# Performance work log

Hardware: AMD Instinct MI355X
Metric: run time of the kernel (lower is better)

## Reference

```python
import jax, jax.numpy as jnp
import numpy as np

N = 20000      # nodes
E = 320000     # edges (before self loops)
HID = 128      # args.hidden
HEADS = 8
C1 = HID // 2  # 64, gat1 out per head -> 512 concat
C2 = HID // 4  # 32, gat2 out per head -> 256 concat
D1 = HEADS * C1  # 512
D2 = HEADS * C2  # 256
JKD = HID + D1 + D2  # 896


def _glorot(key, shape):
    fan_in, fan_out = shape[0], shape[-1]
    s = jnp.sqrt(6.0 / (fan_in + fan_out))
    return jax.random.uniform(key, shape, jnp.float32, -s, s)


def setup_inputs() -> dict:
    key = jax.random.key(0)
    ks = jax.random.split(key, 18)
    x = jax.random.normal(ks[0], (N, HID), jnp.float32)
    edge_index = jax.random.randint(ks[1], (2, E), 0, N, dtype=jnp.int32)
    return {
        "x": x,
        "edge_index": edge_index,
        # GATv2 layer 1
        "Wl1": _glorot(ks[2], (HID, D1)), "bl1": jnp.zeros((D1,), jnp.float32),
        "Wr1": _glorot(ks[3], (HID, D1)), "br1": jnp.zeros((D1,), jnp.float32),
        "att1": _glorot(ks[4], (HEADS, C1)),
        "bias1": jnp.zeros((D1,), jnp.float32),
        # GATv2 layer 2
        "Wl2": _glorot(ks[5], (D1, D2)), "bl2": jnp.zeros((D2,), jnp.float32),
        "Wr2": _glorot(ks[6], (D1, D2)), "br2": jnp.zeros((D2,), jnp.float32),
        "att2": _glorot(ks[7], (HEADS, C2)),
        "bias2": jnp.zeros((D2,), jnp.float32),
        # JK linear
        "Wjk": _glorot(ks[8], (JKD, HID)), "bjk": jnp.zeros((HID,), jnp.float32),
    }


def gatv2_layer(x, src, dst, Wl, bl, Wr, br, att, bias, n):
    """PyG GATv2Conv (concat=True, eval mode: no dropout), neg_slope=0.2."""
    H, C = att.shape
    xl = (x @ Wl + bl).reshape(n, H, C)  # source transform (messages)
    xr = (x @ Wr + br).reshape(n, H, C)  # target transform
    e = jax.nn.leaky_relu(xl[src] + xr[dst], 0.2)        # [E,H,C]
    logits = jnp.einsum('ehc,hc->eh', e, att)            # [E,H]
    # numerically stable segment softmax over incoming edges per dst node
    m = jax.ops.segment_max(logits, dst, num_segments=n) # [N,H]
    a = jnp.exp(logits - m[dst])
    denom = jax.ops.segment_sum(a, dst, num_segments=n)
    alpha = a / denom[dst]                               # [E,H]
    out = jax.ops.segment_sum(alpha[:, :, None] * xl[src], dst, num_segments=n)
    return out.reshape(n, H * C) + bias


def reference(x, edge_index, Wl1, bl1, Wr1, br1, att1, bias1,
              Wl2, bl2, Wr2, br2, att2, bias2, Wjk, bjk):
    n = x.shape[0]
    loop = jnp.arange(n, dtype=edge_index.dtype)
    src = jnp.concatenate([edge_index[0], loop])  # add self loops (PyG default)
    dst = jnp.concatenate([edge_index[1], loop])

    jk0 = x
    h1 = jax.nn.elu(gatv2_layer(x, src, dst, Wl1, bl1, Wr1, br1, att1, bias1, n))
    h2 = jax.nn.elu(gatv2_layer(h1, src, dst, Wl2, bl2, Wr2, br2, att2, bias2, n))
    jk = jnp.concatenate([jk0, h1, h2], axis=-1)  # JumpingKnowledge('cat')
    return jk @ Wjk + bjk
```

## Files before the change

### kernel.cpp

```cpp
#include <hip/hip_runtime.h>

typedef unsigned short u16;
typedef __attribute__((ext_vector_type(8))) short bf16x8;
typedef __attribute__((ext_vector_type(4))) float f32x4;

__device__ __forceinline__ float bf2f(u16 u) { return __uint_as_float(((unsigned)u) << 16); }
__device__ __forceinline__ u16 f2bf(float f) {
  unsigned u = __float_as_uint(f);
  u += 0x7fffu + ((u >> 16) & 1u);
  return (u16)(u >> 16);
}
__device__ __forceinline__ void bf2x2(unsigned w, float& lo, float& hi) {
  lo = __uint_as_float(w << 16);
  hi = __uint_as_float(w & 0xffff0000u);
}

__global__ __launch_bounds__(256) void prep_kernel(
    const float* __restrict__ x,
    const float* __restrict__ bl1, const float* __restrict__ br1,
    const float* __restrict__ bl2, const float* __restrict__ br2,
    u16* __restrict__ XH, float* __restrict__ BC1, float* __restrict__ BC2,
    int nx, int total)
{
  int i = blockIdx.x * 256 + threadIdx.x;
  if (i >= total) return;
  if (i < nx) { XH[i] = f2bf(x[i]); return; }
  int j = i - nx;
  if (j < 1024) { BC1[j] = (j < 512) ? bl1[j] : br1[j - 512]; return; }
  int t = j - 1024;
  BC2[t] = (t < 256) ? bl2[t] : br2[t - 256];
}

__global__ __launch_bounds__(256) void wtrans_kernel(
    const float* __restrict__ Wl1, const float* __restrict__ Wr1,
    const float* __restrict__ Wl2, const float* __restrict__ Wr2,
    const float* __restrict__ Wjk,
    u16* __restrict__ Wp)
{
  __shared__ float T[64][65];
  int t = blockIdx.x;
  const float *Wa, *Wb; int Nhalf, lds, k0, n0, KsT, SUBS; size_t obase; bool split;
  if (t < 32) {
    int kt = t & 1, nt = t >> 1;
    k0 = kt * 64; n0 = nt * 64; obase = 0; KsT = 4; SUBS = 8; split = true;
    Wa = Wl1; Wb = Wr1; Nhalf = 512; lds = 512;
  } else if (t < 96) {
    int tt = t - 32; int kt = tt & 7, nt = tt >> 3;
    k0 = kt * 64; n0 = nt * 64; obase = 262144; KsT = 16; SUBS = 8; split = true;
    Wa = Wl2; Wb = Wr2; Nhalf = 256; lds = 256;
  } else {
    int tt = t - 96; int kt = tt % 14, nt = tt / 14;
    k0 = kt * 64; n0 = nt * 64; obase = 786432; KsT = 28; SUBS = 4; split = false;
    Wa = Wjk; Wb = nullptr; Nhalf = 128; lds = 128;
  }
  const int tid = threadIdx.x;
  const int lane = tid & 63, unit = tid >> 6;
  {
    int n = n0 + lane;
    const float* S = (n < Nhalf) ? Wa : Wb;
    int nn = (n < Nhalf) ? n : n - Nhalf;
#pragma unroll
    for (int r = 0; r < 16; ++r) {
      int kl = unit + 4 * r;
      T[kl][lane] = S[(size_t)(k0 + kl) * lds + nn];
    }
  }
  __syncthreads();
  const int tn = n0 >> 6;
#pragma unroll
  for (int u = 0; u < 2; ++u) {
    int c = unit * 2 + u;
    int ks_l = c >> 2, nc = c & 3;
    int ksg = (k0 >> 5) + ks_l;
    size_t ob = obase + ((size_t)(tn * KsT + ksg) * SUBS + nc) * 512 + lane * 8;
#pragma unroll
    for (int j = 0; j < 8; ++j) {
      float v = T[ks_l * 32 + (lane >> 4) * 8 + j][nc * 16 + (lane & 15)];
      u16 h = f2bf(v);
      Wp[ob + j] = h;
      if (split) Wp[ob + 2048 + j] = f2bf(v - bf2f(h));
    }
  }
}

__global__ __launch_bounds__(256) void hist_kernel(
    const int* __restrict__ ei, int E, int ET, int* __restrict__ cnt)
{
  int e = blockIdx.x * 256 + threadIdx.x;
  if (e >= ET) return;
  int d = (e < E) ? ei[E + e] : (e - E);
  atomicAdd(&cnt[d], 1);
}

__global__ __launch_bounds__(1024) void scan_kernel(
    const int* __restrict__ cnt, int* __restrict__ rowptr, int n)
{
  __shared__ int wsum[16];
  __shared__ int carry;
  const int tid = threadIdx.x, lane = tid & 63, wv = tid >> 6;
  if (tid == 0) carry = 0;
  __syncthreads();
  for (int base = 0; base < n; base += 1024) {
    int i = base + tid;
    int v = (i < n) ? cnt[i] : 0;
    int s = v;
#pragma unroll
    for (int ofs = 1; ofs < 64; ofs <<= 1) {
      int t = __shfl_up(s, ofs);
      if (lane >= ofs) s += t;
    }
    if (lane == 63) wsum[wv] = s;
    __syncthreads();
    if (wv == 0 && lane < 16) {
      int t = wsum[lane];
#pragma unroll
      for (int ofs = 1; ofs < 16; ofs <<= 1) {
        int u = __shfl_up(t, ofs);
        if (lane >= ofs) t += u;
      }
      wsum[lane] = t;
    }
    __syncthreads();
    int waveoff = (wv == 0) ? 0 : wsum[wv - 1];
    if (i < n) rowptr[i] = carry + waveoff + s - v;
    int tot = wsum[15];
    __syncthreads();
    if (tid == 0) carry += tot;
    __syncthreads();
  }
  if (threadIdx.x == 0) rowptr[n] = carry;
}

__global__ __launch_bounds__(256) void scatter_kernel(
    const int* __restrict__ ei, int E, int ET,
    const int* __restrict__ rowptr, int* __restrict__ cur, int* __restrict__ srcs)
{
  int e = blockIdx.x * 256 + threadIdx.x;
  if (e >= ET) return;
  int s, d;
  if (e < E) { s = ei[e]; d = ei[E + e]; } else { s = e - E; d = s; }
  int pos = rowptr[d] + atomicAdd(&cur[d], 1);
  srcs[pos] = s;
}

template<int MROWS, int NW, int WPE, bool SPLIT, bool BF16OUT, int LDSU16>
__global__ __launch_bounds__(NW * 64, WPE) void gemmct_kernel(
    const u16* __restrict__ A0, int lda0, int K0,
    const u16* __restrict__ A1, int lda1, int K1,
    const u16* __restrict__ A2, int lda2, int K2,
    const u16* __restrict__ Wp, int KsT,
    int kof0, int kof1, int kof2,
    const float* __restrict__ bias,
    void* __restrict__ Cv, int ldc, int M, int N)
{
  constexpr int SUBS = SPLIT ? 8 : 4;
  __shared__ u16 ldsA[LDSU16];
  const int tid  = threadIdx.x;
  const int lane = tid & 63;
  const int wv   = tid >> 6;
  const int quad = lane >> 4;
  const int r16  = lane & 15;
  const int m0   = blockIdx.x * MROWS;

  const u16* As[3]   = {A0, A1, A2};
  const int  Ks[3]   = {K0, K1, K2};
  const int  ldas[3] = {lda0, lda1, lda2};
  const int  kofs[3] = {kof0, kof1, kof2};

  int soff[3];
  int so = 0;
#pragma unroll
  for (int s = 0; s < 3; ++s) {
    const int K = Ks[s];
    soff[s] = so;
    if (K == 0) continue;
    const int stride = K + 8;
    const int cpr = K >> 3;
    const int sh  = 32 - __clz(cpr - 1);
    const int tot = MROWS << sh;
    for (int c = tid; c < tot; c += NW * 64) {
      int row = c >> sh, kc = c & ((1 << sh) - 1);
      if (kc < cpr) {
        int sr = m0 + row; if (sr >= M) sr = M - 1;
        uint4 v = *reinterpret_cast<const uint4*>(As[s] + (size_t)sr * ldas[s] + kc * 8);
        *reinterpret_cast<uint4*>(&ldsA[so + row * stride + kc * 8]) = v;
      }
    }
    so += MROWS * stride;
  }
  __syncthreads();

  constexpr int MM = MROWS / 16;
  for (int n0w = wv * 64; n0w < N; n0w += NW * 64) {
    const int t = n0w >> 6;
    f32x4 acc[MM][4];
#pragma unroll
    for (int mm = 0; mm < MM; ++mm)
#pragma unroll
      for (int nc = 0; nc < 4; ++nc) acc[mm][nc] = (f32x4){0.f, 0.f, 0.f, 0.f};

#pragma unroll
    for (int s = 0; s < 3; ++s) {
      const int K = Ks[s];
      if (K == 0) continue;
      const int stride = K + 8;
      const int ksb = kofs[s] >> 5;
      const u16* lbase = &ldsA[soff[s] + r16 * stride + quad * 8];

#pragma unroll 2
      for (int k0 = 0; k0 < K; k0 += 32) {
        const int ks = ksb + (k0 >> 5);
        const u16* ch = Wp + (((size_t)(t * KsT + ks) * SUBS) << 9) + lane * 8;
        bf16x8 af[MM];
#pragma unroll
        for (int mm = 0; mm < MM; ++mm)
          af[mm] = *reinterpret_cast<const bf16x8*>(lbase + mm * 16 * stride + k0);
        bf16x8 whf[4], wlf[4];
#pragma unroll
        for (int nc = 0; nc < 4; ++nc) {
          whf[nc] = *reinterpret_cast<const bf16x8*>(ch + (nc << 9));
          if (SPLIT) wlf[nc] = *reinterpret_cast<const bf16x8*>(ch + ((4 + nc) << 9));
        }
#pragma unroll
        for (int mm = 0; mm < MM; ++mm)
#pragma unroll
          for (int nc = 0; nc < 4; ++nc) {
            acc[mm][nc] = __builtin_amdgcn_mfma_f32_16x16x32_bf16(whf[nc], af[mm], acc[mm][nc], 0, 0, 0);
            if (SPLIT)
              acc[mm][nc] = __builtin_amdgcn_mfma_f32_16x16x32_bf16(wlf[nc], af[mm], acc[mm][nc], 0, 0, 0);
          }
      }
    }

#pragma unroll
    for (int mm = 0; mm < MM; ++mm) {
      const int m = m0 + mm * 16 + r16;
      if (m >= M) continue;
#pragma unroll
      for (int nc = 0; nc < 4; ++nc) {
        const int n = n0w + nc * 16 + quad * 4;
        float b0 = 0.f, b1 = 0.f, b2 = 0.f, b3 = 0.f;
        if (bias) {
          float4 bv = *reinterpret_cast<const float4*>(bias + n);
          b0 = bv.x; b1 = bv.y; b2 = bv.z; b3 = bv.w;
        }
        float v0 = acc[mm][nc][0] + b0;
        float v1 = acc[mm][nc][1] + b1;
        float v2 = acc[mm][nc][2] + b2;
        float v3 = acc[mm][nc][3] + b3;
        if (BF16OUT) {
          ushort4 o = { f2bf(v0), f2bf(v1), f2bf(v2), f2bf(v3) };
          *reinterpret_cast<ushort4*>((u16*)Cv + (size_t)m * ldc + n) = o;
        } else {
          float4 o = { v0, v1, v2, v3 };
          *reinterpret_cast<float4*>((float*)Cv + (size_t)m * ldc + n) = o;
        }
      }
    }
  }
}

template<int VPL>
__device__ __forceinline__ void load_row(const u16* p, float* dst) {
  if constexpr (VPL == 8) {
    uint4 t = *reinterpret_cast<const uint4*>(p);
    bf2x2(t.x, dst[0], dst[1]); bf2x2(t.y, dst[2], dst[3]);
    bf2x2(t.z, dst[4], dst[5]); bf2x2(t.w, dst[6], dst[7]);
  } else {
    uint2 t = *reinterpret_cast<const uint2*>(p);
    bf2x2(t.x, dst[0], dst[1]); bf2x2(t.y, dst[2], dst[3]);
  }
}

template<int C>
__global__ __launch_bounds__(256) void gat_node_kernel(
    const u16* __restrict__ XLR,
    const int* __restrict__ rowptr, const int* __restrict__ srcs,
    const float* __restrict__ att, const float* __restrict__ bias,
    u16* __restrict__ Hh, int Nn)
{
  constexpr int D = C * 8;
  constexpr int VPL = D / 64;
  const int lane = threadIdx.x & 63;
  const int wv  = (blockIdx.x * 256 + threadIdx.x) >> 6;
  const int nwv = (gridDim.x * 256) >> 6;

  float c1[VPL], c2[VPL], biasR[VPL];
#pragma unroll
  for (int w = 0; w < VPL; ++w) {
    float a = att[lane * VPL + w];
    c1[w] = 0.6f * a;
    c2[w] = 0.4f * a;
    biasR[w] = bias[lane * VPL + w];
  }

  for (int d = wv; d < Nn; d += nwv) {
    float xr[VPL];
    load_row<VPL>(XLR + (size_t)d * (2 * D) + D + lane * VPL, xr);

    const int jb = rowptr[d], je = rowptr[d + 1];

    float acc[VPL];
    load_row<VPL>(XLR + (size_t)srcs[jb] * (2 * D) + lane * VPL, acc);
    float p0 = 0.f;
#pragma unroll
    for (int w = 0; w < VPL; ++w) {
      float v = acc[w] + xr[w];
      p0 = fmaf(c1[w], v, fmaf(c2[w], fabsf(v), p0));
    }
    p0 += __shfl_xor(p0, 1);
    p0 += __shfl_xor(p0, 2);
    p0 += __shfl_xor(p0, 4);
    float den = 1.f;

    int j = jb + 1;
    for (; j + 1 < je; j += 2) {
      float xa[VPL], xb[VPL];
      load_row<VPL>(XLR + (size_t)srcs[j]     * (2 * D) + lane * VPL, xa);
      load_row<VPL>(XLR + (size_t)srcs[j + 1] * (2 * D) + lane * VPL, xb);
      float pa = 0.f, pb = 0.f;
#pragma unroll
      for (int w = 0; w < VPL; ++w) {
        float va = xa[w] + xr[w];
        float vb = xb[w] + xr[w];
        pa = fmaf(c1[w], va, fmaf(c2[w], fabsf(va), pa));
        pb = fmaf(c1[w], vb, fmaf(c2[w], fabsf(vb), pb));
      }
      pa += __shfl_xor(pa, 1); pb += __shfl_xor(pb, 1);
      pa += __shfl_xor(pa, 2); pb += __shfl_xor(pb, 2);
      pa += __shfl_xor(pa, 4); pb += __shfl_xor(pb, 4);
      const float ea = __expf(pa - p0);
      const float eb = __expf(pb - p0);
      den += ea + eb;
#pragma unroll
      for (int w = 0; w < VPL; ++w)
        acc[w] = fmaf(ea, xa[w], fmaf(eb, xb[w], acc[w]));
    }
    if (j < je) {
      float xa[VPL];
      load_row<VPL>(XLR + (size_t)srcs[j] * (2 * D) + lane * VPL, xa);
      float pa = 0.f;
#pragma unroll
      for (int w = 0; w < VPL; ++w) {
        float va = xa[w] + xr[w];
        pa = fmaf(c1[w], va, fmaf(c2[w], fabsf(va), pa));
      }
      pa += __shfl_xor(pa, 1);
      pa += __shfl_xor(pa, 2);
      pa += __shfl_xor(pa, 4);
      const float ea = __expf(pa - p0);
      den += ea;
#pragma unroll
      for (int w = 0; w < VPL; ++w) acc[w] = fmaf(ea, xa[w], acc[w]);
    }

    const float inv = 1.f / den;
    u16* hh = Hh + (size_t)d * D + lane * VPL;
#pragma unroll
    for (int w = 0; w < VPL; ++w) {
      float v = fmaf(acc[w], inv, biasR[w]);
      v = v > 0.f ? v : (__expf(v) - 1.f);
      hh[w] = f2bf(v);
    }
  }
}


extern "C" void kernel_launch(void* const* d_in, const int* in_sizes, int n_in,
                              void* d_out, int out_size, void* d_ws, size_t ws_size,
                              hipStream_t stream) {
  const float* x     = (const float*)d_in[0];
  const int*   ei    = (const int*)d_in[1];
  const float* Wl1   = (const float*)d_in[2];
  const float* bl1   = (const float*)d_in[3];
  const float* Wr1   = (const float*)d_in[4];
  const float* br1   = (const float*)d_in[5];
  const float* att1  = (const float*)d_in[6];
  const float* bias1 = (const float*)d_in[7];
  const float* Wl2   = (const float*)d_in[8];
  const float* bl2   = (const float*)d_in[9];
  const float* Wr2   = (const float*)d_in[10];
  const float* br2   = (const float*)d_in[11];
  const float* att2  = (const float*)d_in[12];
  const float* bias2 = (const float*)d_in[13];
  const float* Wjk   = (const float*)d_in[14];
  const float* bjk   = (const float*)d_in[15];
  float* out = (float*)d_out;

  const int Nn = in_sizes[0] / 128;
  const int E  = in_sizes[1] / 2;
  const int ET = E + Nn;

  const size_t nx = (size_t)Nn * 128;

  const size_t oW1  = 0;
  const size_t oW2  = 262144;
  const size_t oWjk = 786432;
  const size_t npack = 901120;

  char* ws = (char*)d_ws;
  size_t off = 0;
  u16* XH = (u16*)(ws + off); off += nx * 2;
  u16* Wp = (u16*)(ws + off); off += npack * 2;
  float* BC1 = (float*)(ws + off); off += 1024 * 4;
  float* BC2 = (float*)(ws + off); off += 512 * 4;
  u16* XLR1 = (u16*)(ws + off);
  u16* XLR2 = XLR1;
  off += (size_t)Nn * 1024 * 2;
  u16* H1h = (u16*)(ws + off); off += (size_t)Nn * 512 * 2;
  u16* H2h = (u16*)(ws + off); off += (size_t)Nn * 256 * 2;
  int* rowptr = (int*)(ws + off); off += (size_t)(Nn + 1) * 4;
  int* cur    = (int*)(ws + off); off += (size_t)Nn * 4;
  int* srcs   = (int*)(ws + off); off += (size_t)ET * 4;

  const int nodeblocks = 1250;

  const int nprep = (int)(nx + 1536);
  prep_kernel<<<(nprep + 255) / 256, 256, 0, stream>>>(
      x, bl1, br1, bl2, br2, XH, BC1, BC2, (int)nx, nprep);
  wtrans_kernel<<<124, 256, 0, stream>>>(Wl1, Wr1, Wl2, Wr2, Wjk, Wp);
  hipMemsetAsync(cur, 0, (size_t)Nn * 4, stream);
  hist_kernel<<<(ET + 255) / 256, 256, 0, stream>>>(ei, E, ET, cur);
  scan_kernel<<<1, 1024, 0, stream>>>(cur, rowptr, Nn);
  hipMemsetAsync(cur, 0, (size_t)Nn * 4, stream);
  scatter_kernel<<<(ET + 255) / 256, 256, 0, stream>>>(ei, E, ET, rowptr, cur, srcs);

  gemmct_kernel<32, 8, 4, true, true, 32 * 136>
      <<<(Nn + 31) / 32, 512, 0, stream>>>(
      XH, 128, 128, nullptr, 0, 0, nullptr, 0, 0,
      Wp + oW1, 4, 0, 0, 0, BC1,
      XLR1, 1024, Nn, 1024);
  gat_node_kernel<64><<<nodeblocks, 256, 0, stream>>>(
      XLR1, rowptr, srcs, att1, bias1, H1h, Nn);

  gemmct_kernel<48, 8, 4, true, true, 48 * 520>
      <<<(Nn + 47) / 48, 512, 0, stream>>>(
      H1h, 512, 512, nullptr, 0, 0, nullptr, 0, 0,
      Wp + oW2, 16, 0, 0, 0, BC2,
      XLR2, 512, Nn, 512);
  gat_node_kernel<32><<<nodeblocks, 256, 0, stream>>>(
      XLR2, rowptr, srcs, att2, bias2, H2h, Nn);

  gemmct_kernel<16, 2, 1, false, false, 16 * 920>
      <<<(Nn + 15) / 16, 128, 0, stream>>>(
      XH, 128, 128, H1h, 512, 512, H2h, 256, 256,
      Wp + oWjk, 28, 0, 128, 640, bjk,
      out, 128, Nn, 128);
}
```

Baseline: 340.3 us.

## Balance GAT node waves by edge count and vectorize math with packed float2

Adds a partition kernel that binary-searches rowptr so each of 5000 waves covers a contiguous node range holding roughly equal numbers of edges. The old grid-stride loop assigned nodes round-robin without regard to degree. The GAT node kernel also switches to float2 vector arithmetic, which can map to packed FP32 instructions, and computes leaky-relu as max(v, 0.2v). The cost is an extra small kernel launch, and contiguous node ranges change the memory access pattern.

Result: slower. 352.4 us (+3.6%).

```diff
diff --git a/kernel.cpp b/kernel.cpp
--- a/kernel.cpp
+++ b/kernel.cpp
@@ -3,6 +3,7 @@
 typedef unsigned short u16;
 typedef __attribute__((ext_vector_type(8))) short bf16x8;
 typedef __attribute__((ext_vector_type(4))) float f32x4;
+typedef __attribute__((ext_vector_type(2))) float f32x2;
 
 __device__ __forceinline__ float bf2f(u16 u) { return __uint_as_float(((unsigned)u) << 16); }
 __device__ __forceinline__ u16 f2bf(float f) {
@@ -10,9 +11,11 @@
   u += 0x7fffu + ((u >> 16) & 1u);
   return (u16)(u >> 16);
 }
-__device__ __forceinline__ void bf2x2(unsigned w, float& lo, float& hi) {
-  lo = __uint_as_float(w << 16);
-  hi = __uint_as_float(w & 0xffff0000u);
+__device__ __forceinline__ f32x2 bf2v(unsigned w) {
+  f32x2 r;
+  r.x = __uint_as_float(w << 16);
+  r.y = __uint_as_float(w & 0xffff0000u);
+  return r;
 }
 
 __global__ __launch_bounds__(256) void prep_kernel(
@@ -141,6 +144,20 @@
   if (e < E) { s = ei[e]; d = ei[E + e]; } else { s = e - E; d = s; }
   int pos = rowptr[d] + atomicAdd(&cur[d], 1);
   srcs[pos] = s;
+}
+
+__global__ __launch_bounds__(256) void partition_kernel(
+    const int* __restrict__ rowptr, int Nn, int ET, int nw, int* __restrict__ wbeg)
+{
+  int w = blockIdx.x * 256 + threadIdx.x;
+  if (w > nw) return;
+  long long target = (long long)ET * w / nw;
+  int lo = 0, hi = Nn;
+  while (lo < hi) {
+    int mid = (lo + hi + 1) >> 1;
+    if ((long long)rowptr[mid] <= target) lo = mid; else hi = mid - 1;
+  }
+  wbeg[w] = lo;
 }
 
 template<int MROWS, int NW, int WPE, bool SPLIT, bool BF16OUT, int LDSU16>
@@ -260,15 +277,14 @@
   }
 }
 
-template<int VPL>
-__device__ __forceinline__ void load_row(const u16* p, float* dst) {
-  if constexpr (VPL == 8) {
+template<int NV2>
+__device__ __forceinline__ void load_row2(const u16* p, f32x2* dst) {
+  if constexpr (NV2 == 4) {
     uint4 t = *reinterpret_cast<const uint4*>(p);
-    bf2x2(t.x, dst[0], dst[1]); bf2x2(t.y, dst[2], dst[3]);
-    bf2x2(t.z, dst[4], dst[5]); bf2x2(t.w, dst[6], dst[7]);
+    dst[0] = bf2v(t.x); dst[1] = bf2v(t.y); dst[2] = bf2v(t.z); dst[3] = bf2v(t.w);
   } else {
     uint2 t = *reinterpret_cast<const uint2*>(p);
-    bf2x2(t.x, dst[0], dst[1]); bf2x2(t.y, dst[2], dst[3]);
+    dst[0] = bf2v(t.x); dst[1] = bf2v(t.y);
   }
 }
 
@@ -277,37 +293,41 @@
     const u16* __restrict__ XLR,
     const int* __restrict__ rowptr, const int* __restrict__ srcs,
     const float* __restrict__ att, const float* __restrict__ bias,
-    u16* __restrict__ Hh, int Nn)
+    u16* __restrict__ Hh, const int* __restrict__ wbeg, int nwaves)
 {
   constexpr int D = C * 8;
   constexpr int VPL = D / 64;
+  constexpr int NV2 = VPL / 2;
   const int lane = threadIdx.x & 63;
   const int wv  = (blockIdx.x * 256 + threadIdx.x) >> 6;
-  const int nwv = (gridDim.x * 256) >> 6;
-
-  float c1[VPL], c2[VPL], biasR[VPL];
-#pragma unroll
-  for (int w = 0; w < VPL; ++w) {
-    float a = att[lane * VPL + w];
-    c1[w] = 0.6f * a;
-    c2[w] = 0.4f * a;
-    biasR[w] = bias[lane * VPL + w];
-  }
-
-  for (int d = wv; d < Nn; d += nwv) {
-    float xr[VPL];
-    load_row<VPL>(XLR + (size_t)d * (2 * D) + D + lane * VPL, xr);
+  if (wv >= nwaves) return;
+
+  f32x2 attR[NV2], biasR[NV2];
+#pragma unroll
+  for (int w = 0; w < NV2; ++w) {
+    attR[w].x  = att[lane * VPL + 2 * w];
+    attR[w].y  = att[lane * VPL + 2 * w + 1];
+    biasR[w].x = bias[lane * VPL + 2 * w];
+    biasR[w].y = bias[lane * VPL + 2 * w + 1];
+  }
+
+  const int dbeg = wbeg[wv], dend = wbeg[wv + 1];
+  for (int d = dbeg; d < dend; ++d) {
+    f32x2 xr[NV2];
+    load_row2<NV2>(XLR + (size_t)d * (2 * D) + D + lane * VPL, xr);
 
     const int jb = rowptr[d], je = rowptr[d + 1];
 
-    float acc[VPL];
-    load_row<VPL>(XLR + (size_t)srcs[jb] * (2 * D) + lane * VPL, acc);
-    float p0 = 0.f;
-#pragma unroll
-    for (int w = 0; w < VPL; ++w) {
-      float v = acc[w] + xr[w];
-      p0 = fmaf(c1[w], v, fmaf(c2[w], fabsf(v), p0));
-    }
+    f32x2 acc[NV2];
+    load_row2<NV2>(XLR + (size_t)srcs[jb] * (2 * D) + lane * VPL, acc);
+    f32x2 p02 = {0.f, 0.f};
+#pragma unroll
+    for (int w = 0; w < NV2; ++w) {
+      f32x2 va = acc[w] + xr[w];
+      f32x2 vm = __builtin_elementwise_max(va, 0.2f * va);
+      p02 += attR[w] * vm;
+    }
+    float p0 = p02.x + p02.y;
     p0 += __shfl_xor(p0, 1);
     p0 += __shfl_xor(p0, 2);
     p0 += __shfl_xor(p0, 4);
@@ -315,52 +335,62 @@
 
     int j = jb + 1;
     for (; j + 1 < je; j += 2) {
-      float xa[VPL], xb[VPL];
-      load_row<VPL>(XLR + (size_t)srcs[j]     * (2 * D) + lane * VPL, xa);
-      load_row<VPL>(XLR + (size_t)srcs[j + 1] * (2 * D) + lane * VPL, xb);
-      float pa = 0.f, pb = 0.f;
-#pragma unroll
-      for (int w = 0; w < VPL; ++w) {
-        float va = xa[w] + xr[w];
-        float vb = xb[w] + xr[w];
-        pa = fmaf(c1[w], va, fmaf(c2[w], fabsf(va), pa));
-        pb = fmaf(c1[w], vb, fmaf(c2[w], fabsf(vb), pb));
-      }
+      f32x2 xa[NV2], xb[NV2];
+      load_row2<NV2>(XLR + (size_t)srcs[j]     * (2 * D) + lane * VPL, xa);
+      load_row2<NV2>(XLR + (size_t)srcs[j + 1] * (2 * D) + lane * VPL, xb);
+      f32x2 pa2 = {0.f, 0.f}, pb2 = {0.f, 0.f};
+#pragma unroll
+      for (int w = 0; w < NV2; ++w) {
+        f32x2 va = xa[w] + xr[w];
+        f32x2 vb = xb[w] + xr[w];
+        f32x2 vam = __builtin_elementwise_max(va, 0.2f * va);
+        f32x2 vbm = __builtin_elementwise_max(vb, 0.2f * vb);
+        pa2 += attR[w] * vam;
+        pb2 += attR[w] * vbm;
+      }
+      float pa = pa2.x + pa2.y, pb = pb2.x + pb2.y;
       pa += __shfl_xor(pa, 1); pb += __shfl_xor(pb, 1);
       pa += __shfl_xor(pa, 2); pb += __shfl_xor(pb, 2);
       pa += __shfl_xor(pa, 4); pb += __shfl_xor(pb, 4);
       const float ea = __expf(pa - p0);
       const float eb = __expf(pb - p0);
       den += ea + eb;
-#pragma unroll
-      for (int w = 0; w < VPL; ++w)
-        acc[w] = fmaf(ea, xa[w], fmaf(eb, xb[w], acc[w]));
+      const f32x2 ea2 = {ea, ea}, eb2 = {eb, eb};
+#pragma unroll
+      for (int w = 0; w < NV2; ++w)
+        acc[w] += ea2 * xa[w] + eb2 * xb[w];
     }
     if (j < je) {
-      float xa[VPL];
-      load_row<VPL>(XLR + (size_t)srcs[j] * (2 * D) + lane * VPL, xa);
-      float pa = 0.f;
-#pragma unroll
-      for (int w = 0; w < VPL; ++w) {
-        float va = xa[w] + xr[w];
-        pa = fmaf(c1[w], va, fmaf(c2[w], fabsf(va), pa));
-      }
+      f32x2 xa[NV2];
+      load_row2<NV2>(XLR + (size_t)srcs[j] * (2 * D) + lane * VPL, xa);
+      f32x2 pa2 = {0.f, 0.f};
+#pragma unroll
+      for (int w = 0; w < NV2; ++w) {
+        f32x2 va = xa[w] + xr[w];
+        f32x2 vam = __builtin_elementwise_max(va, 0.2f * va);
+        pa2 += attR[w] * vam;
+      }
+      float pa = pa2.x + pa2.y;
       pa += __shfl_xor(pa, 1);
       pa += __shfl_xor(pa, 2);
       pa += __shfl_xor(pa, 4);
       const float ea = __expf(pa - p0);
       den += ea;
-#pragma unroll
-      for (int w = 0; w < VPL; ++w) acc[w] = fmaf(ea, xa[w], acc[w]);
+      const f32x2 ea2 = {ea, ea};
+#pragma unroll
+      for (int w = 0; w < NV2; ++w) acc[w] += ea2 * xa[w];
     }
 
     const float inv = 1.f / den;
+    const f32x2 inv2 = {inv, inv};
     u16* hh = Hh + (size_t)d * D + lane * VPL;
 #pragma unroll
-    for (int w = 0; w < VPL; ++w) {
-      float v = fmaf(acc[w], inv, biasR[w]);
-      v = v > 0.f ? v : (__expf(v) - 1.f);
-      hh[w] = f2bf(v);
+    for (int w = 0; w < NV2; ++w) {
+      f32x2 v = acc[w] * inv2 + biasR[w];
+      float v0 = v.x > 0.f ? v.x : (__expf(v.x) - 1.f);
+      float v1 = v.y > 0.f ? v.y : (__expf(v.y) - 1.f);
+      hh[2 * w]     = f2bf(v0);
+      hh[2 * w + 1] = f2bf(v1);
     }
   }
 }
@@ -398,6 +428,8 @@
   const size_t oWjk = 786432;
   const size_t npack = 901120;
 
+  const int NWAVES = 5000;
+
   char* ws = (char*)d_ws;
   size_t off = 0;
   u16* XH = (u16*)(ws + off); off += nx * 2;
@@ -412,8 +444,9 @@
   int* rowptr = (int*)(ws + off); off += (size_t)(Nn + 1) * 4;
   int* cur    = (int*)(ws + off); off += (size_t)Nn * 4;
   int* srcs   = (int*)(ws + off); off += (size_t)ET * 4;
-
-  const int nodeblocks = 1250;
+  int* wbeg   = (int*)(ws + off); off += (size_t)(NWAVES + 1) * 4;
+
+  const int nodeblocks = NWAVES / 4;
 
   const int nprep = (int)(nx + 1536);
   prep_kernel<<<(nprep + 255) / 256, 256, 0, stream>>>(
@@ -422,6 +455,8 @@
   hipMemsetAsync(cur, 0, (size_t)Nn * 4, stream);
   hist_kernel<<<(ET + 255) / 256, 256, 0, stream>>>(ei, E, ET, cur);
   scan_kernel<<<1, 1024, 0, stream>>>(cur, rowptr, Nn);
+  partition_kernel<<<(NWAVES + 256) / 256, 256, 0, stream>>>(
+      rowptr, Nn, ET, NWAVES, wbeg);
   hipMemsetAsync(cur, 0, (size_t)Nn * 4, stream);
   scatter_kernel<<<(ET + 255) / 256, 256, 0, stream>>>(ei, E, ET, rowptr, cur, srcs);
 
@@ -431,7 +466,7 @@
       Wp + oW1, 4, 0, 0, 0, BC1,
       XLR1, 1024, Nn, 1024);
   gat_node_kernel<64><<<nodeblocks, 256, 0, stream>>>(
-      XLR1, rowptr, srcs, att1, bias1, H1h, Nn);
+      XLR1, rowptr, srcs, att1, bias1, H1h, wbeg, NWAVES);
 
   gemmct_kernel<48, 8, 4, true, true, 48 * 520>
       <<<(Nn + 47) / 48, 512, 0, stream>>>(
@@ -439,7 +474,7 @@
       Wp + oW2, 16, 0, 0, 0, BC2,
       XLR2, 512, Nn, 512);
   gat_node_kernel<32><<<nodeblocks, 256, 0, stream>>>(
-      XLR2, rowptr, srcs, att2, bias2, H2h, Nn);
+      XLR2, rowptr, srcs, att2, bias2, H2h, wbeg, NWAVES);
 
   gemmct_kernel<16, 2, 1, false, false, 16 * 920>
       <<<(Nn + 15) / 16, 128, 0, stream>>>(
```
